# Performance work log

Hardware: AMD Instinct MI355X
Metric: run time of the kernel (lower is better)

## Reference

```python
import jax, jax.numpy as jnp
import numpy as np

BETA = 2
KERAS_EPS = 1e-7  # keras.backend.epsilon()


def _masks(n):
    idx = np.arange(n)
    # eps2[i,j] = 1 iff i<j  (itertools.combinations for N=2)
    eps2 = (idx[:, None] < idx[None, :]).astype(np.float32)
    # eps3[i,j,k] = 1 iff i<j<k  (itertools.combinations for N=3)
    eps3 = ((idx[:, None, None] < idx[None, :, None])
            & (idx[None, :, None] < idx[None, None, :])).astype(np.float32)
    return jnp.asarray(eps2), jnp.asarray(eps3)


def _jet_ecf(x, beta):
    # x: [B, n, 3] = (pt, eta, phi)
    n = x.shape[1]
    pt = x[:, :, 0]    # [B, n]
    eta = x[:, :, 1]
    phi = x[:, :, 2]
    # pairwise squared distance in (eta, phi): [B, n, n]
    R2 = (eta[:, :, None] - eta[:, None, :]) ** 2 \
       + (phi[:, :, None] - phi[:, None, :]) ** 2
    if beta == 2:
        Rb = R2
    elif beta == 1:
        Rb = jnp.sqrt(R2)
    else:
        Rb = R2 ** (beta / 2)

    eps2, eps3 = _masks(n)

    ecf1 = jnp.sum(pt, axis=-1, keepdims=True)                         # [B, 1]
    ecf2 = jnp.einsum('ij,ai,aj,aij->a', eps2, pt, pt, Rb)[:, None]    # [B, 1]
    ecf3 = jnp.einsum('ijk,ai,aj,ak,aij,aik,ajk->a',
                      eps3, pt, pt, pt, Rb, Rb, Rb)[:, None]           # [B, 1]
    return ecf1, ecf2, ecf3


def setup_inputs() -> dict:
    key = jax.random.key(0)
    x = jax.random.normal(key, (2048, 200, 3), dtype=jnp.float32)
    return {"x": x}


def reference(x):
    ecf1, ecf2, ecf3 = _jet_ecf(x, BETA)
    d2 = ecf3 * ecf1 ** 3 / (ecf2 ** 3 + KERAS_EPS)
    return jnp.concatenate([ecf1, ecf2, ecf3, d2], axis=-1)  # [B, 4]
```

## Files before the change

### kernel.cpp

```cpp
#include <hip/hip_runtime.h>


constexpr int NPART = 200;

__device__ __forceinline__ float bcast(float v, int ii) {
    return __int_as_float(__builtin_amdgcn_readlane(__float_as_int(v), ii));
}

__global__ __launch_bounds__(64) void jet_ecf_kernel(const float* __restrict__ x,
                                                     float* __restrict__ out,
                                                     int njet) {
#pragma clang fp contract(off)
    const int jet = blockIdx.x;
    if (jet >= njet) return;
    const int lane = threadIdx.x;
    const float* xj = x + (size_t)jet * NPART * 3;

    float pw[4], pe[4], pp[4];
    {
        const int base[4] = { 0, 8, 72, 136 };
        #pragma unroll
        for (int k = 0; k < 4; ++k) {
            const int p = base[k] + lane;
            const bool valid = (k > 0) || (lane < 8);
            if (valid) {
                pw[k] = xj[p * 3 + 0];
                pe[k] = xj[p * 3 + 1];
                pp[k] = xj[p * 3 + 2];
            } else {
                pw[k] = 0.0f; pe[k] = 0.0f; pp[k] = 0.0f;
            }
        }
    }

    double S = 0, Sa = 0, Se = 0, Sp = 0, Saa = 0;
    double Sae = 0, Sap = 0, See = 0, Spp = 0, Sep = 0;
    #pragma unroll
    for (int k = 0; k < 4; ++k) {
        const double w = (double)pw[k];
        const double e = (double)pe[k];
        const double f = (double)pp[k];
        const double a = e * e + f * f;
        S   += w;        Sa  += w * a;     Se  += w * e;
        Sp  += w * f;    Saa += w * a * a; Sae += w * a * e;
        Sap += w * a * f; See += w * e * e; Spp += w * f * f;
        Sep += w * e * f;
    }
    #pragma unroll
    for (int off = 32; off > 0; off >>= 1) {
        S   += __shfl_down(S,   off, 64);
        Sa  += __shfl_down(Sa,  off, 64);
        Se  += __shfl_down(Se,  off, 64);
        Sp  += __shfl_down(Sp,  off, 64);
        Saa += __shfl_down(Saa, off, 64);
        Sae += __shfl_down(Sae, off, 64);
        Sap += __shfl_down(Sap, off, 64);
        See += __shfl_down(See, off, 64);
        Spp += __shfl_down(Spp, off, 64);
        Sep += __shfl_down(Sep, off, 64);
    }

    float s0 = 0.0f, s1 = 0.0f, s2 = 0.0f, s3 = 0.0f;

#define BODY(ACC, K)                                                          \
    {                                                                         \
        const float de = __fsub_rn(ei, pe[K]);                                \
        const float dp = __fsub_rn(pi, pp[K]);                                \
        const float r2 = __fadd_rn(__fmul_rn(de, de), __fmul_rn(dp, dp));     \
        ACC = __fadd_rn(ACC, __fmul_rn(r2, wi));                              \
    }
#define BODY_PRED(ACC, K)                                                     \
    {                                                                         \
        const float de = __fsub_rn(ei, pe[K]);                                \
        const float dp = __fsub_rn(pi, pp[K]);                                \
        const float r2 = __fadd_rn(__fmul_rn(de, de), __fmul_rn(dp, dp));     \
        const float c  = __fmul_rn(r2, wi);                                   \
        ACC = __fadd_rn(ACC, (ii < lane) ? c : 0.0f);                         \
    }
#define LOAD_I(I)                                                             \
    const float wi = xj[3 * (I) + 0];                                         \
    const float ei = xj[3 * (I) + 1];                                         \
    const float pi = xj[3 * (I) + 2];

    #pragma unroll
    for (int ii = 0; ii < 7; ++ii) {
        LOAD_I(ii)
        BODY_PRED(s0, 0)
        BODY(s1, 1)
        BODY(s2, 2)
        BODY(s3, 3)
    }
    {
        const int ii = 7;
        LOAD_I(ii)
        BODY(s1, 1)
        BODY(s2, 2)
        BODY(s3, 3)
    }
    #pragma unroll 4
    for (int ii = 0; ii < 63; ++ii) {
        LOAD_I(8 + ii)
        BODY_PRED(s1, 1)
        BODY(s2, 2)
        BODY(s3, 3)
    }
    {
        const int ii = 71;
        LOAD_I(ii)
        BODY(s2, 2)
        BODY(s3, 3)
    }
    #pragma unroll 4
    for (int ii = 0; ii < 63; ++ii) {
        LOAD_I(72 + ii)
        BODY_PRED(s2, 2)
        BODY(s3, 3)
    }
    {
        const int ii = 135;
        LOAD_I(ii)
        BODY(s3, 3)
    }
    #pragma unroll 4
    for (int ii = 0; ii < 63; ++ii) {
        LOAD_I(136 + ii)
        BODY_PRED(s3, 3)
    }
#undef BODY
#undef BODY_PRED
#undef LOAD_I

    const float t0 = __fmul_rn(pw[0], s0);
    const float t1 = __fmul_rn(pw[1], s1);
    const float t2 = __fmul_rn(pw[2], s2);
    const float t3 = __fmul_rn(pw[3], s3);

    float e2f = 0.0f;
    #pragma unroll
    for (int ii = 0; ii < 8; ++ii)  e2f = __fadd_rn(e2f, bcast(t0, ii));
    #pragma unroll 8
    for (int ii = 0; ii < 64; ++ii) e2f = __fadd_rn(e2f, bcast(t1, ii));
    #pragma unroll 8
    for (int ii = 0; ii < 64; ++ii) e2f = __fadd_rn(e2f, bcast(t2, ii));
    #pragma unroll 8
    for (int ii = 0; ii < 64; ++ii) e2f = __fadd_rn(e2f, bcast(t3, ii));

    if (lane == 0) {
        const double A[4][4] = {
            {  Saa,        Sa,       -2.0 * Sae, -2.0 * Sap },
            {  Sa,         S,        -2.0 * Se,  -2.0 * Sp  },
            { -2.0 * Sae, -2.0 * Se,  4.0 * See,  4.0 * Sep },
            { -2.0 * Sap, -2.0 * Sp,  4.0 * Sep,  4.0 * Spp }
        };
        const double B[4][4] = {
            { Sa,  S,  -2.0 * Se,  -2.0 * Sp  },
            { Saa, Sa, -2.0 * Sae, -2.0 * Sap },
            { Sae, Se, -2.0 * See, -2.0 * Sep },
            { Sap, Sp, -2.0 * Sep, -2.0 * Spp }
        };
        const double C[4][4] = {
            { S,  Sa,  Se,  Sp  },
            { Sa, Saa, Sae, Sap },
            { Se, Sae, See, Sep },
            { Sp, Sap, Sep, Spp }
        };
        double T = 0.0;
        #pragma unroll
        for (int b = 0; b < 4; ++b) {
            #pragma unroll
            for (int g = 0; g < 4; ++g) {
                double ab = 0.0;
                #pragma unroll
                for (int al = 0; al < 4; ++al) ab += A[al][b] * B[al][g];
                T += ab * C[b][g];
            }
        }
        const double ecf1 = S;
        const double ecf2 = (double)e2f;
        const double ecf3 = T * (1.0 / 6.0);
        const double d2 = ecf3 * ecf1 * ecf1 * ecf1 / (ecf2 * ecf2 * ecf2 + 1e-7);
        float4 o = make_float4((float)ecf1, (float)ecf2, (float)ecf3, (float)d2);
        *reinterpret_cast<float4*>(out + (size_t)jet * 4) = o;
    }
}

extern "C" void kernel_launch(void* const* d_in, const int* in_sizes, int n_in,
                              void* d_out, int out_size, void* d_ws, size_t ws_size,
                              hipStream_t stream) {
    const float* x = (const float*)d_in[0];
    float* out = (float*)d_out;
    const int njet = in_sizes[0] / (NPART * 3);
    jet_ecf_kernel<<<njet, 64, 0, stream>>>(x, out, njet);
}
```

Baseline: 72.52 us.

## Stage jet particles in LDS and run a packed-FP32 software-pipelined pair loop

```diff
diff --git a/kernel.cpp b/kernel.cpp
--- a/kernel.cpp
+++ b/kernel.cpp
@@ -2,9 +2,142 @@
 
 
 constexpr int NPART = 200;
+typedef float f2 __attribute__((ext_vector_type(2)));
 
 __device__ __forceinline__ float bcast(float v, int ii) {
     return __int_as_float(__builtin_amdgcn_readlane(__float_as_int(v), ii));
+}
+
+constexpr int offA(int g) {
+    return (g < 72) ? g : (g == 135 ? 135 : g - 64);
+}
+
+struct Ctx {
+    f2 bw[5], be[5], bp[5];
+    f2 acc23, accY, tt;
+    f2 pe01, pp01, pe23, pp23, pe13, pp13, n1;
+    float a0, a1, a2, a3;
+    float pe1, pp1, pe3, pp3;
+    unsigned aw, ae, ap;
+    int lane;
+};
+
+template <int G>
+__device__ __forceinline__ void prefetch(Ctx& c) {
+    constexpr int A = offA(G), B = G, S = G % 5;
+    asm volatile(
+        "ds_read2_b32 %[w], %[aw] offset0:%c[A] offset1:%c[B]\n\t"
+        "ds_read2_b32 %[e], %[ae] offset0:%c[A] offset1:%c[B]\n\t"
+        "ds_read2_b32 %[p], %[ap] offset0:%c[A] offset1:%c[B]\n\t"
+        : [w] "+v"(c.bw[S]), [e] "+v"(c.be[S]), [p] "+v"(c.bp[S])
+        : [aw] "v"(c.aw), [ae] "v"(c.ae), [ap] "v"(c.ap), [A] "i"(A), [B] "i"(B));
+}
+
+template <int G>
+__device__ __forceinline__ void cstep(Ctx& c) {
+    constexpr int rem = 198 - G;
+    constexpr int K = 3 * (rem < 4 ? rem : 4);
+    constexpr int S = G % 5;
+    if constexpr (G <= 6) {
+        f2 t1, t2;
+        asm volatile(
+            "s_waitcnt lgkmcnt(%c[K])\n\t"
+            "v_pk_fma_f32 %[t1], %[pe01], %[n1], %[be]\n\t"
+            "v_pk_fma_f32 %[t2], %[pp01], %[n1], %[bp]\n\t"
+            "v_pk_mul_f32 %[t1], %[t1], %[t1]\n\t"
+            "v_pk_mul_f32 %[t2], %[t2], %[t2]\n\t"
+            "v_pk_add_f32 %[t1], %[t1], %[t2]\n\t"
+            "v_pk_mul_f32 %[tt], %[t1], %[bw]\n\t"
+            "v_pk_fma_f32 %[t1], %[pe23], %[n1], %[be]\n\t"
+            "v_pk_fma_f32 %[t2], %[pp23], %[n1], %[bp]\n\t"
+            "v_pk_mul_f32 %[t1], %[t1], %[t1]\n\t"
+            "v_pk_mul_f32 %[t2], %[t2], %[t2]\n\t"
+            "v_pk_add_f32 %[t1], %[t1], %[t2]\n\t"
+            "v_pk_mul_f32 %[t1], %[t1], %[bw]\n\t"
+            "v_pk_add_f32 %[acc], %[acc], %[t1]\n\t"
+            : [t1] "=&v"(t1), [t2] "=&v"(t2), [tt] "=&v"(c.tt),
+              [acc] "+v"(c.acc23), [bw] "+v"(c.bw[S]), [be] "+v"(c.be[S]),
+              [bp] "+v"(c.bp[S])
+            : [pe01] "v"(c.pe01), [pp01] "v"(c.pp01), [pe23] "v"(c.pe23),
+              [pp23] "v"(c.pp23), [n1] "v"(c.n1), [K] "i"(K));
+        c.a1 = __fadd_rn(c.a1, c.tt.y);
+        c.a0 = __fadd_rn(c.a0, (G < c.lane) ? c.tt.x : 0.0f);
+    } else if constexpr (G <= 71) {
+        f2 t1, t2;
+        asm volatile(
+            "s_waitcnt lgkmcnt(%c[K])\n\t"
+            "v_pk_fma_f32 %[t1], %[pe23], %[n1], %[be]\n\t"
+            "v_pk_fma_f32 %[t2], %[pp23], %[n1], %[bp]\n\t"
+            "v_pk_mul_f32 %[t1], %[t1], %[t1]\n\t"
+            "v_pk_mul_f32 %[t2], %[t2], %[t2]\n\t"
+            "v_pk_add_f32 %[t1], %[t1], %[t2]\n\t"
+            "v_pk_mul_f32 %[t1], %[t1], %[bw]\n\t"
+            "v_pk_add_f32 %[acc], %[acc], %[t1]\n\t"
+            : [t1] "=&v"(t1), [t2] "=&v"(t2), [acc] "+v"(c.acc23),
+              [bw] "+v"(c.bw[S]), [be] "+v"(c.be[S]), [bp] "+v"(c.bp[S])
+            : [pe23] "v"(c.pe23), [pp23] "v"(c.pp23), [n1] "v"(c.n1), [K] "i"(K));
+        if constexpr (G == 7) {
+            const float de = __fsub_rn(c.be[S].x, c.pe1);
+            const float dp = __fsub_rn(c.bp[S].x, c.pp1);
+            const float r2 = __fadd_rn(__fmul_rn(de, de), __fmul_rn(dp, dp));
+            c.a1 = __fadd_rn(c.a1, __fmul_rn(r2, c.bw[S].x));
+        }
+    } else if constexpr (G <= 134) {
+        if constexpr (G == 72) { c.a2 = c.acc23.x; c.a3 = c.acc23.y; }
+        f2 t1, t2;
+        asm volatile(
+            "s_waitcnt lgkmcnt(%c[K])\n\t"
+            "v_pk_fma_f32 %[t1], %[pe13], %[n1], %[be]\n\t"
+            "v_pk_fma_f32 %[t2], %[pp13], %[n1], %[bp]\n\t"
+            "v_pk_mul_f32 %[t1], %[t1], %[t1]\n\t"
+            "v_pk_mul_f32 %[t2], %[t2], %[t2]\n\t"
+            "v_pk_add_f32 %[t1], %[t1], %[t2]\n\t"
+            "v_pk_mul_f32 %[tt], %[t1], %[bw]\n\t"
+            : [t1] "=&v"(t1), [t2] "=&v"(t2), [tt] "=&v"(c.tt),
+              [bw] "+v"(c.bw[S]), [be] "+v"(c.be[S]), [bp] "+v"(c.bp[S])
+            : [pe13] "v"(c.pe13), [pp13] "v"(c.pp13), [n1] "v"(c.n1), [K] "i"(K));
+        c.a3 = __fadd_rn(c.a3, c.tt.y);
+        c.a1 = __fadd_rn(c.a1, ((G - 72) < c.lane) ? c.tt.x : 0.0f);
+    } else if constexpr (G == 135) {
+        asm volatile("s_waitcnt lgkmcnt(%c[K])"
+                     : [bw] "+v"(c.bw[S]), [be] "+v"(c.be[S]), [bp] "+v"(c.bp[S])
+                     : [K] "i"(K));
+        const float de = __fsub_rn(c.be[S].x, c.pe3);
+        const float dp = __fsub_rn(c.bp[S].x, c.pp3);
+        const float r2 = __fadd_rn(__fmul_rn(de, de), __fmul_rn(dp, dp));
+        c.a3 = __fadd_rn(c.a3, __fmul_rn(r2, c.bw[S].x));
+    } else {
+        if constexpr (G == 136) { c.accY.x = c.a2; c.accY.y = c.a3; }
+        constexpr unsigned sh = G - 135;
+        constexpr unsigned lm = sh < 32 ? (0xFFFFFFFFu << sh) : 0u;
+        constexpr unsigned hm = sh < 32 ? 0xFFFFFFFFu : (0xFFFFFFFFu << (sh - 32));
+        f2 t1, t2;
+        asm volatile(
+            "s_waitcnt lgkmcnt(%c[K])\n\t"
+            "s_mov_b32 exec_lo, %c[LM]\n\t"
+            "s_mov_b32 exec_hi, %c[HM]\n\t"
+            "v_pk_fma_f32 %[t1], %[pe23], %[n1], %[be]\n\t"
+            "v_pk_fma_f32 %[t2], %[pp23], %[n1], %[bp]\n\t"
+            "v_pk_mul_f32 %[t1], %[t1], %[t1]\n\t"
+            "v_pk_mul_f32 %[t2], %[t2], %[t2]\n\t"
+            "v_pk_add_f32 %[t1], %[t1], %[t2]\n\t"
+            "v_pk_mul_f32 %[t1], %[t1], %[bw]\n\t"
+            "v_pk_add_f32 %[acc], %[acc], %[t1]\n\t"
+            "s_mov_b64 exec, -1\n\t"
+            : [t1] "=&v"(t1), [t2] "=&v"(t2), [acc] "+v"(c.accY),
+              [bw] "+v"(c.bw[S]), [be] "+v"(c.be[S]), [bp] "+v"(c.bp[S])
+            : [pe23] "v"(c.pe23), [pp23] "v"(c.pp23), [n1] "v"(c.n1),
+              [K] "i"(K), [LM] "i"(lm), [HM] "i"(hm));
+    }
+}
+
+template <int G>
+__device__ __forceinline__ void run(Ctx& c) {
+    if constexpr (G <= 198) {
+        cstep<G>(c);
+        if constexpr (G + 5 <= 198) prefetch<G + 5>(c);
+        run<G + 1>(c);
+    }
 }
 
 __global__ __launch_bounds__(64) void jet_ecf_kernel(const float* __restrict__ x,
@@ -16,30 +149,42 @@
     const int lane = threadIdx.x;
     const float* xj = x + (size_t)jet * NPART * 3;
 
-    float pw[4], pe[4], pp[4];
+    __shared__ float lds[600];
+
+    float pw[4], pea[4], ppa[4];
     {
-        const int base[4] = { 0, 8, 72, 136 };
+        const int base[4] = {0, 8, 72, 136};
         #pragma unroll
         for (int k = 0; k < 4; ++k) {
             const int p = base[k] + lane;
             const bool valid = (k > 0) || (lane < 8);
             if (valid) {
                 pw[k] = xj[p * 3 + 0];
-                pe[k] = xj[p * 3 + 1];
-                pp[k] = xj[p * 3 + 2];
+                pea[k] = xj[p * 3 + 1];
+                ppa[k] = xj[p * 3 + 2];
             } else {
-                pw[k] = 0.0f; pe[k] = 0.0f; pp[k] = 0.0f;
+                pw[k] = 0.0f; pea[k] = 0.0f; ppa[k] = 0.0f;
             }
         }
     }
 
+    #pragma unroll
+    for (int r = 0; r < 4; ++r) {
+        const int i = lane + (r << 6);
+        if (i < NPART) {
+            lds[i]       = xj[3 * i + 0];
+            lds[200 + i] = xj[3 * i + 1];
+            lds[400 + i] = xj[3 * i + 2];
+        }
+    }
+
     double S = 0, Sa = 0, Se = 0, Sp = 0, Saa = 0;
     double Sae = 0, Sap = 0, See = 0, Spp = 0, Sep = 0;
     #pragma unroll
     for (int k = 0; k < 4; ++k) {
         const double w = (double)pw[k];
-        const double e = (double)pe[k];
-        const double f = (double)pp[k];
+        const double e = (double)pea[k];
+        const double f = (double)ppa[k];
         const double a = e * e + f * f;
         S   += w;        Sa  += w * a;     Se  += w * e;
         Sp  += w * f;    Saa += w * a * a; Sae += w * a * e;
@@ -60,80 +205,45 @@
         Sep += __shfl_down(Sep, off, 64);
     }
 
-    float s0 = 0.0f, s1 = 0.0f, s2 = 0.0f, s3 = 0.0f;
-
-#define BODY(ACC, K)                                                          \
-    {                                                                         \
-        const float de = __fsub_rn(ei, pe[K]);                                \
-        const float dp = __fsub_rn(pi, pp[K]);                                \
-        const float r2 = __fadd_rn(__fmul_rn(de, de), __fmul_rn(dp, dp));     \
-        ACC = __fadd_rn(ACC, __fmul_rn(r2, wi));                              \
-    }
-#define BODY_PRED(ACC, K)                                                     \
-    {                                                                         \
-        const float de = __fsub_rn(ei, pe[K]);                                \
-        const float dp = __fsub_rn(pi, pp[K]);                                \
-        const float r2 = __fadd_rn(__fmul_rn(de, de), __fmul_rn(dp, dp));     \
-        const float c  = __fmul_rn(r2, wi);                                   \
-        ACC = __fadd_rn(ACC, (ii < lane) ? c : 0.0f);                         \
-    }
-#define LOAD_I(I)                                                             \
-    const float wi = xj[3 * (I) + 0];                                         \
-    const float ei = xj[3 * (I) + 1];                                         \
-    const float pi = xj[3 * (I) + 2];
-
-    #pragma unroll
-    for (int ii = 0; ii < 7; ++ii) {
-        LOAD_I(ii)
-        BODY_PRED(s0, 0)
-        BODY(s1, 1)
-        BODY(s2, 2)
-        BODY(s3, 3)
-    }
-    {
-        const int ii = 7;
-        LOAD_I(ii)
-        BODY(s1, 1)
-        BODY(s2, 2)
-        BODY(s3, 3)
-    }
-    #pragma unroll 4
-    for (int ii = 0; ii < 63; ++ii) {
-        LOAD_I(8 + ii)
-        BODY_PRED(s1, 1)
-        BODY(s2, 2)
-        BODY(s3, 3)
-    }
-    {
-        const int ii = 71;
-        LOAD_I(ii)
-        BODY(s2, 2)
-        BODY(s3, 3)
-    }
-    #pragma unroll 4
-    for (int ii = 0; ii < 63; ++ii) {
-        LOAD_I(72 + ii)
-        BODY_PRED(s2, 2)
-        BODY(s3, 3)
-    }
-    {
-        const int ii = 135;
-        LOAD_I(ii)
-        BODY(s3, 3)
-    }
-    #pragma unroll 4
-    for (int ii = 0; ii < 63; ++ii) {
-        LOAD_I(136 + ii)
-        BODY_PRED(s3, 3)
-    }
-#undef BODY
-#undef BODY_PRED
-#undef LOAD_I
-
-    const float t0 = __fmul_rn(pw[0], s0);
-    const float t1 = __fmul_rn(pw[1], s1);
-    const float t2 = __fmul_rn(pw[2], s2);
-    const float t3 = __fmul_rn(pw[3], s3);
+    __syncthreads();
+    asm volatile("" ::: "memory");
+    asm volatile("" :: "v"(S), "v"(Sa), "v"(Se), "v"(Sp), "v"(Saa),
+                       "v"(Sae), "v"(Sap), "v"(See), "v"(Spp), "v"(Sep));
+    __builtin_amdgcn_sched_barrier(0);
+    asm volatile("s_waitcnt lgkmcnt(0)" ::: );
+
+    Ctx c;
+    c.lane = lane;
+    c.aw = (unsigned)(uintptr_t)&lds[0];
+    c.ae = (unsigned)(uintptr_t)&lds[200];
+    c.ap = (unsigned)(uintptr_t)&lds[400];
+    c.n1.x = -1.0f; c.n1.y = -1.0f;
+    c.pe01.x = pea[0]; c.pe01.y = pea[1];
+    c.pp01.x = ppa[0]; c.pp01.y = ppa[1];
+    c.pe23.x = pea[2]; c.pe23.y = pea[3];
+    c.pp23.x = ppa[2]; c.pp23.y = ppa[3];
+    c.pe13.x = pea[1]; c.pe13.y = pea[3];
+    c.pp13.x = ppa[1]; c.pp13.y = ppa[3];
+    c.pe1 = pea[1]; c.pp1 = ppa[1]; c.pe3 = pea[3]; c.pp3 = ppa[3];
+    c.acc23.x = 0.0f; c.acc23.y = 0.0f;
+    c.accY.x = 0.0f;  c.accY.y = 0.0f;
+    c.tt.x = 0.0f;    c.tt.y = 0.0f;
+    c.a0 = c.a1 = c.a2 = c.a3 = 0.0f;
+    #pragma unroll
+    for (int k = 0; k < 5; ++k) {
+        c.bw[k].x = 0.0f; c.bw[k].y = 0.0f;
+        c.be[k].x = 0.0f; c.be[k].y = 0.0f;
+        c.bp[k].x = 0.0f; c.bp[k].y = 0.0f;
+    }
+
+    prefetch<0>(c); prefetch<1>(c); prefetch<2>(c); prefetch<3>(c); prefetch<4>(c);
+    run<0>(c);
+    c.a2 = c.accY.x; c.a3 = c.accY.y;
+
+    const float t0 = __fmul_rn(pw[0], c.a0);
+    const float t1 = __fmul_rn(pw[1], c.a1);
+    const float t2 = __fmul_rn(pw[2], c.a2);
+    const float t3 = __fmul_rn(pw[3], c.a3);
 
     float e2f = 0.0f;
     #pragma unroll
```

Result: faster. 70.69 us (-2.5%).
